# Kernel optimization log

Hardware: AMD Instinct MI355X
Metric: run time of the kernel (lower is better)

The kernel has to match this reference:

```python
import jax, jax.numpy as jnp
import numpy as np

B, N, D, D_A, S, D_K = 512, 8192, 1024, 512, 8, 64

def setup_inputs() -> dict:
    key = jax.random.key(0)
    k1, k2, k3, k4 = jax.random.split(key, 4)
    lecun_q = 1.0 / np.sqrt(D_A)
    lecun_k = 1.0 / np.sqrt(D)
    return {
        "z": jax.random.normal(k1, (B, D_A), dtype=jnp.float32),
        "pool_vectors": jax.random.normal(k2, (N, D), dtype=jnp.float32),
        "W_Q": jax.random.normal(k3, (S, D_A, D_K), dtype=jnp.float32) * lecun_q,
        "W_K": jax.random.normal(k4, (S, D, D_K), dtype=jnp.float32) * lecun_k,
        "aspect_logits": jnp.zeros((S,), dtype=jnp.float32),
        "tau": jnp.asarray(0.5, dtype=jnp.float32),
        "lambda_sharp": jnp.asarray(10.0, dtype=jnp.float32),
        "temperature": jnp.asarray(0.1, dtype=jnp.float32),
    }

def reference(z, pool_vectors, W_Q, W_K, aspect_logits, tau, lambda_sharp, temperature):
    # Per-aspect projections
    queries = jnp.einsum('bd,adq->baq', z, W_Q)              # [B, S, d_k]
    keys = jnp.einsum('np,apq->naq', pool_vectors, W_K)       # [N, S, d_k]
    # L2 normalize along d_k
    q_norm = queries / (jnp.linalg.norm(queries, axis=-1, keepdims=True) + 1e-08)
    k_norm = keys / (jnp.linalg.norm(keys, axis=-1, keepdims=True) + 1e-08)
    # Multi-aspect cosine similarity
    sims = jnp.einsum('baq,naq->bna', q_norm, k_norm)          # [B, N, S]
    # Learned aspect weighting
    w = jax.nn.softmax(aspect_logits)                          # [S]
    scores = jnp.einsum('bna,a->bn', sims, w)                  # [B, N]
    # Sigmoid gate against threshold, temperature-scaled normalize
    g = jax.nn.sigmoid(lambda_sharp * (scores - tau))
    alpha_raw = g * jnp.exp(scores / temperature)
    alpha = alpha_raw / (jnp.sum(alpha_raw, axis=-1, keepdims=True) + 1e-08)
    return (alpha, scores, keys)
```

## Files before the change

kernel.cpp:

```cpp
#include <hip/hip_runtime.h>
#include <stdint.h>

#define B_DIM 512
#define N_DIM 8192
#define D_DIM 1024
#define DA_DIM 512
#define S_DIM 8
#define DK_DIM 64
#define C_DIM 512

typedef short v8s __attribute__((ext_vector_type(8)));
typedef float v4f __attribute__((ext_vector_type(4)));

__device__ __forceinline__ unsigned int f2bf(float x) {
    union { float f; unsigned int u; } v; v.f = x;
    unsigned int u = v.u;
    return (u + 0x7fffu + ((u >> 16) & 1u)) >> 16;
}

__device__ __forceinline__ void gld16(const unsigned short* g, unsigned short* l) {
    __builtin_amdgcn_global_load_lds(
        (const __attribute__((address_space(1))) unsigned int*)g,
        (__attribute__((address_space(3))) unsigned int*)l,
        16, 0, 0);
}

__device__ __forceinline__ void cvt8(const float* __restrict__ src,
                                     unsigned short* __restrict__ dst, int t) {
    const float4* s4 = (const float4*)src;
    float4 a = s4[2 * t], b = s4[2 * t + 1];
    uint4 o;
    o.x = f2bf(a.x) | (f2bf(a.y) << 16);
    o.y = f2bf(a.z) | (f2bf(a.w) << 16);
    o.z = f2bf(b.x) | (f2bf(b.y) << 16);
    o.w = f2bf(b.z) | (f2bf(b.w) << 16);
    ((uint4*)dst)[t] = o;
}

__device__ __forceinline__ void w_transpose(const float* __restrict__ w,
                                            unsigned short* __restrict__ wt,
                                            int c, int ddim) {
    int a = c >> 6, k = c & 63;
    const float* src = w + (size_t)a * ddim * DK_DIM + k;
    unsigned short* drow = wt + (size_t)c * ddim;
    for (int d = threadIdx.x; d < ddim; d += 256)
        drow[d] = (unsigned short)f2bf(src[(size_t)d * DK_DIM]);
}

__global__ __launch_bounds__(256) void prep(const float* __restrict__ pool,
                                            const float* __restrict__ z,
                                            const float* __restrict__ W_Q,
                                            const float* __restrict__ W_K,
                                            unsigned short* __restrict__ poolb,
                                            unsigned short* __restrict__ zb,
                                            unsigned short* __restrict__ wqt,
                                            unsigned short* __restrict__ wtb) {
    int blk = blockIdx.x;
    if (blk < 4096) {
        cvt8(pool, poolb, blk * 256 + threadIdx.x);
    } else if (blk < 4224) {
        cvt8(z, zb, (blk - 4096) * 256 + threadIdx.x);
    } else if (blk < 4736) {
        w_transpose(W_K, wtb, blk - 4224, D_DIM);
    } else {
        w_transpose(W_Q, wqt, blk - 4736, DA_DIM);
    }
}

__device__ __forceinline__ void gemm_mainloop(const unsigned short* __restrict__ A, int lda,
                                              const unsigned short* __restrict__ Bm, int ldb,
                                              int mbase, int nbase, int kiters,
                                              unsigned short* As, unsigned short* Bs,
                                              v4f acc[4][4]) {
    int tid = threadIdx.x;
    int wid = tid >> 6, lane = tid & 63;
    int wm = wid >> 1, wn = wid & 1;
    int quad = lane >> 4, l16 = lane & 15;
    int srow = lane >> 2;
    int scol = (lane & 3) * 8;

    for (int kk = 0; kk < kiters; kk++) {
        #pragma unroll
        for (int j = 0; j < 2; j++) {
            int rgrp = wid * 2 + j;
            int row = rgrp * 16 + srow;
            gld16(&A[(size_t)(mbase + row) * lda + kk * 32 + scol], &As[rgrp * 512]);
            gld16(&Bm[(size_t)(nbase + row) * ldb + kk * 32 + scol], &Bs[rgrp * 512]);
        }
        __syncthreads();
        v8s af[4], bf[4];
        #pragma unroll
        for (int mt = 0; mt < 4; mt++)
            af[mt] = *(const v8s*)&As[(wm * 64 + mt * 16 + l16) * 32 + quad * 8];
        #pragma unroll
        for (int nt = 0; nt < 4; nt++)
            bf[nt] = *(const v8s*)&Bs[(wn * 64 + nt * 16 + l16) * 32 + quad * 8];
        #pragma unroll
        for (int mt = 0; mt < 4; mt++)
            #pragma unroll
            for (int nt = 0; nt < 4; nt++)
                acc[mt][nt] = __builtin_amdgcn_mfma_f32_16x16x32_bf16(
                    af[mt], bf[nt], acc[mt][nt], 0, 0, 0);
        __syncthreads();
    }
}

__global__ __launch_bounds__(256) void fused_gemms(const unsigned short* __restrict__ poolb,
                                                   const unsigned short* __restrict__ wtb,
                                                   const unsigned short* __restrict__ zb,
                                                   const unsigned short* __restrict__ wqt,
                                                   const float* __restrict__ logits,
                                                   float* __restrict__ keys_out,
                                                   unsigned short* __restrict__ kb,
                                                   unsigned short* __restrict__ qwb) {
    __shared__ unsigned short As[4096], Bs[4096];
    v4f acc[4][4];
    #pragma unroll
    for (int mt = 0; mt < 4; mt++)
        #pragma unroll
        for (int nt = 0; nt < 4; nt++) acc[mt][nt] = (v4f)(0.f);

    int blk = blockIdx.x;
    bool is_q = blk >= 256;
    const unsigned short* A;
    const unsigned short* Bm;
    int lda, mbase, nbase, kiters;
    if (is_q) {
        int q = blk - 256;
        A = zb; Bm = wqt; lda = DA_DIM; kiters = DA_DIM / 32;
        mbase = (q >> 2) * 128; nbase = (q & 3) * 128;
    } else {
        A = poolb; Bm = wtb; lda = D_DIM; kiters = D_DIM / 32;
        mbase = (blk >> 2) * 128; nbase = (blk & 3) * 128;
    }

    gemm_mainloop(A, lda, Bm, lda, mbase, nbase, kiters, As, Bs, acc);

    int tid = threadIdx.x, wid = tid >> 6, lane = tid & 63;
    int wm = wid >> 1, wn = wid & 1, quad = lane >> 4, l16 = lane & 15;

    if (is_q) {
        float l[8]; float mx = -1e30f;
        #pragma unroll
        for (int i = 0; i < 8; i++) { l[i] = logits[i]; mx = fmaxf(mx, l[i]); }
        float se = 0.f;
        #pragma unroll
        for (int i = 0; i < 8; i++) { l[i] = __expf(l[i] - mx); se += l[i]; }
        float wa = l[(nbase >> 6) + wn] / se;

        #pragma unroll
        for (int mt = 0; mt < 4; mt++)
            #pragma unroll
            for (int r = 0; r < 4; r++) {
                float ss = 0.f;
                #pragma unroll
                for (int nt = 0; nt < 4; nt++) {
                    float s = acc[mt][nt][r];
                    ss += s * s;
                }
                ss += __shfl_xor(ss, 1, 64);
                ss += __shfl_xor(ss, 2, 64);
                ss += __shfl_xor(ss, 4, 64);
                ss += __shfl_xor(ss, 8, 64);
                float sc = wa / (sqrtf(ss) + 1e-8f);
                int row = mbase + wm * 64 + mt * 16 + quad * 4 + r;
                #pragma unroll
                for (int nt = 0; nt < 4; nt++) {
                    int col = nbase + wn * 64 + nt * 16 + l16;
                    qwb[(size_t)row * C_DIM + col] =
                        (unsigned short)f2bf(acc[mt][nt][r] * sc);
                }
            }
    } else {
        #pragma unroll
        for (int mt = 0; mt < 4; mt++)
            #pragma unroll
            for (int r = 0; r < 4; r++) {
                float ss = 0.f;
                #pragma unroll
                for (int nt = 0; nt < 4; nt++) {
                    float s = acc[mt][nt][r];
                    ss += s * s;
                }
                ss += __shfl_xor(ss, 1, 64);
                ss += __shfl_xor(ss, 2, 64);
                ss += __shfl_xor(ss, 4, 64);
                ss += __shfl_xor(ss, 8, 64);
                float sc = 1.0f / (sqrtf(ss) + 1e-8f);
                int row = mbase + wm * 64 + mt * 16 + quad * 4 + r;
                #pragma unroll
                for (int nt = 0; nt < 4; nt++) {
                    int col = nbase + wn * 64 + nt * 16 + l16;
                    float s = acc[mt][nt][r];
                    keys_out[(size_t)row * C_DIM + col] = s;
                    kb[(size_t)row * C_DIM + col] = (unsigned short)f2bf(s * sc);
                }
            }
    }
}

__global__ __launch_bounds__(256) void scores_gemm(const unsigned short* __restrict__ qwb,
                                                   const unsigned short* __restrict__ kb,
                                                   float* __restrict__ scores_out,
                                                   float* __restrict__ partials,
                                                   const float* __restrict__ lam_p,
                                                   const float* __restrict__ tau_p,
                                                   const float* __restrict__ temp_p) {
    __shared__ unsigned short As[4096], Bs[4096];
    __shared__ float rowpart[128];
    v4f acc[4][4];
    #pragma unroll
    for (int mt = 0; mt < 4; mt++)
        #pragma unroll
        for (int nt = 0; nt < 4; nt++) acc[mt][nt] = (v4f)(0.f);

    int mbase = blockIdx.y * 128, nbase = blockIdx.x * 128;
    gemm_mainloop(qwb, C_DIM, kb, C_DIM, mbase, nbase, C_DIM / 32, As, Bs, acc);

    int tid = threadIdx.x, wid = tid >> 6, lane = tid & 63;
    int wm = wid >> 1, wn = wid & 1, quad = lane >> 4, l16 = lane & 15;

    if (tid < 128) rowpart[tid] = 0.f;
    __syncthreads();

    float lam = lam_p[0], tau = tau_p[0], invT = 1.0f / temp_p[0];
    float rsum[4][4];
    #pragma unroll
    for (int mt = 0; mt < 4; mt++)
        #pragma unroll
        for (int r = 0; r < 4; r++) rsum[mt][r] = 0.f;

    #pragma unroll
    for (int mt = 0; mt < 4; mt++)
        #pragma unroll
        for (int nt = 0; nt < 4; nt++)
            #pragma unroll
            for (int r = 0; r < 4; r++) {
                float s = acc[mt][nt][r];
                int row = mbase + wm * 64 + mt * 16 + quad * 4 + r;
                int col = nbase + wn * 64 + nt * 16 + l16;
                scores_out[(size_t)row * N_DIM + col] = s;
                float g = 1.0f / (1.0f + __expf(-lam * (s - tau)));
                rsum[mt][r] += g * __expf(s * invT);
            }
    #pragma unroll
    for (int mt = 0; mt < 4; mt++)
        #pragma unroll
        for (int r = 0; r < 4; r++) {
            float v = rsum[mt][r];
            v += __shfl_xor(v, 1, 64);
            v += __shfl_xor(v, 2, 64);
            v += __shfl_xor(v, 4, 64);
            v += __shfl_xor(v, 8, 64);
            if (l16 == 0)
                atomicAdd(&rowpart[wm * 64 + mt * 16 + quad * 4 + r], v);
        }
    __syncthreads();
    if (tid < 128)
        partials[(size_t)blockIdx.x * B_DIM + mbase + tid] = rowpart[tid];
}

__global__ __launch_bounds__(256) void alpha_kernel(const float* __restrict__ scores,
                                                    const float* __restrict__ partials,
                                                    float* __restrict__ alpha,
                                                    const float* __restrict__ lam_p,
                                                    const float* __restrict__ tau_p,
                                                    const float* __restrict__ temp_p) {
    __shared__ float s_inv;
    int b = blockIdx.x;
    int tid = threadIdx.x;
    if (tid < 64) {
        float v = partials[(size_t)tid * B_DIM + b];
        v += __shfl_xor(v, 1, 64);
        v += __shfl_xor(v, 2, 64);
        v += __shfl_xor(v, 4, 64);
        v += __shfl_xor(v, 8, 64);
        v += __shfl_xor(v, 16, 64);
        v += __shfl_xor(v, 32, 64);
        if (tid == 0) s_inv = 1.0f / (v + 1e-8f);
    }
    __syncthreads();
    float inv = s_inv;
    float lam = lam_p[0], tau = tau_p[0], invT = 1.0f / temp_p[0];
    const float4* srow = (const float4*)(scores + (size_t)b * N_DIM);
    float4* arow = (float4*)(alpha + (size_t)b * N_DIM);
    #pragma unroll
    for (int i = 0; i < 8; i++) {
        int idx = tid + i * 256;
        float4 s4 = srow[idx];
        float4 o;
        o.x = (1.0f / (1.0f + __expf(-lam * (s4.x - tau)))) * __expf(s4.x * invT) * inv;
        o.y = (1.0f / (1.0f + __expf(-lam * (s4.y - tau)))) * __expf(s4.y * invT) * inv;
        o.z = (1.0f / (1.0f + __expf(-lam * (s4.z - tau)))) * __expf(s4.z * invT) * inv;
        o.w = (1.0f / (1.0f + __expf(-lam * (s4.w - tau)))) * __expf(s4.w * invT) * inv;
        arow[idx] = o;
    }
}

extern "C" void kernel_launch(void* const* d_in, const int* in_sizes, int n_in,
                              void* d_out, int out_size, void* d_ws, size_t ws_size,
                              hipStream_t stream) {
    const float* z      = (const float*)d_in[0];
    const float* pool   = (const float*)d_in[1];
    const float* W_Q    = (const float*)d_in[2];
    const float* W_K    = (const float*)d_in[3];
    const float* logits = (const float*)d_in[4];
    const float* tau    = (const float*)d_in[5];
    const float* lam    = (const float*)d_in[6];
    const float* temp   = (const float*)d_in[7];

    float* alpha  = (float*)d_out;
    float* scores = alpha + (size_t)B_DIM * N_DIM;
    float* keys   = scores + (size_t)B_DIM * N_DIM;

    char* ws = (char*)d_ws;
    unsigned short* poolb = (unsigned short*)(ws);
    unsigned short* kb    = (unsigned short*)(ws + 16777216);
    unsigned short* wtb   = (unsigned short*)(ws + 25165824);
    unsigned short* wqt   = (unsigned short*)(ws + 26214400);
    unsigned short* zb    = (unsigned short*)(ws + 26738688);
    unsigned short* qwb   = (unsigned short*)(ws + 27262976);
    float* partials       = (float*)(ws + 27787264);

    prep<<<dim3(5248), dim3(256), 0, stream>>>(pool, z, W_Q, W_K,
                                               poolb, zb, wqt, wtb);
    fused_gemms<<<dim3(272), dim3(256), 0, stream>>>(poolb, wtb, zb, wqt, logits,
                                                     keys, kb, qwb);
    scores_gemm<<<dim3(64, 4), dim3(256), 0, stream>>>(qwb, kb, scores, partials,
                                                       lam, tau, temp);
    alpha_kernel<<<dim3(512), dim3(256), 0, stream>>>(scores, partials, alpha,
                                                      lam, tau, temp);
}
```

Baseline: 161.2 us.

## Double-buffer GEMM LDS tiles and use tiled shared-memory weight transpose

The GEMM main loop now double-buffers its A/B shared-memory tiles, issuing the next k-slice's global-to-LDS loads before computing on the current slice, with one barrier per iteration instead of two. The weight transpose in the prep kernel becomes a 64x64 tiled transpose through padded shared memory, so global reads and writes are coalesced instead of strided, and the transpose grid shrinks. This doubles GEMM LDS usage, which may lower occupancy. The single barrier per iteration relies on the buffer being overwritten having been consumed in the previous iteration.

```diff
diff --git a/kernel.cpp b/kernel.cpp
--- a/kernel.cpp
+++ b/kernel.cpp
@@ -37,14 +37,39 @@
     ((uint4*)dst)[t] = o;
 }
 
-__device__ __forceinline__ void w_transpose(const float* __restrict__ w,
-                                            unsigned short* __restrict__ wt,
-                                            int c, int ddim) {
-    int a = c >> 6, k = c & 63;
-    const float* src = w + (size_t)a * ddim * DK_DIM + k;
-    unsigned short* drow = wt + (size_t)c * ddim;
-    for (int d = threadIdx.x; d < ddim; d += 256)
-        drow[d] = (unsigned short)f2bf(src[(size_t)d * DK_DIM]);
+__device__ __forceinline__ void w_transpose_tile(const float* __restrict__ w,
+                                                 unsigned short* __restrict__ wt,
+                                                 int a, int dt, int ddim,
+                                                 unsigned short* T ) {
+    int t = threadIdx.x;
+    int d0 = dt * 64;
+    int kc4 = (t & 15) * 4;
+    const float4* src = (const float4*)(w + ((size_t)a * ddim + d0) * DK_DIM);
+    #pragma unroll
+    for (int p = 0; p < 4; p++) {
+        int dr = p * 16 + (t >> 4);
+        float4 v = src[dr * 16 + (t & 15)];
+        uint2 pk;
+        pk.x = f2bf(v.x) | (f2bf(v.y) << 16);
+        pk.y = f2bf(v.z) | (f2bf(v.w) << 16);
+        *(uint2*)&T[dr * 68 + kc4] = pk;
+    }
+    __syncthreads();
+    int c0 = a * 64;
+    #pragma unroll
+    for (int q = 0; q < 2; q++) {
+        int k = q * 32 + (t >> 3);
+        int ch = t & 7;
+        unsigned short s[8];
+        #pragma unroll
+        for (int i = 0; i < 8; i++) s[i] = T[(ch * 8 + i) * 68 + k];
+        uint4 o;
+        o.x = (unsigned)s[0] | ((unsigned)s[1] << 16);
+        o.y = (unsigned)s[2] | ((unsigned)s[3] << 16);
+        o.z = (unsigned)s[4] | ((unsigned)s[5] << 16);
+        o.w = (unsigned)s[6] | ((unsigned)s[7] << 16);
+        *(uint4*)&wt[(size_t)(c0 + k) * ddim + d0 + ch * 8] = o;
+    }
 }
 
 __global__ __launch_bounds__(256) void prep(const float* __restrict__ pool,
@@ -55,22 +80,26 @@
                                             unsigned short* __restrict__ zb,
                                             unsigned short* __restrict__ wqt,
                                             unsigned short* __restrict__ wtb) {
+    __shared__ unsigned short T[64 * 68];
     int blk = blockIdx.x;
     if (blk < 4096) {
         cvt8(pool, poolb, blk * 256 + threadIdx.x);
     } else if (blk < 4224) {
         cvt8(z, zb, (blk - 4096) * 256 + threadIdx.x);
-    } else if (blk < 4736) {
-        w_transpose(W_K, wtb, blk - 4224, D_DIM);
+    } else if (blk < 4352) {
+        int idx = blk - 4224;
+        w_transpose_tile(W_K, wtb, idx >> 4, idx & 15, D_DIM, T);
     } else {
-        w_transpose(W_Q, wqt, blk - 4736, DA_DIM);
+        int idx = blk - 4352;
+        w_transpose_tile(W_Q, wqt, idx >> 3, idx & 7, DA_DIM, T);
     }
 }
 
 __device__ __forceinline__ void gemm_mainloop(const unsigned short* __restrict__ A, int lda,
                                               const unsigned short* __restrict__ Bm, int ldb,
                                               int mbase, int nbase, int kiters,
-                                              unsigned short* As, unsigned short* Bs,
+                                              unsigned short (*As)[4096],
+                                              unsigned short (*Bs)[4096],
                                               v4f acc[4][4]) {
     int tid = threadIdx.x;
     int wid = tid >> 6, lane = tid & 63;
@@ -79,29 +108,34 @@
     int srow = lane >> 2;
     int scol = (lane & 3) * 8;
 
-    for (int kk = 0; kk < kiters; kk++) {
+    auto stage = [&](int kk, int p) {
         #pragma unroll
         for (int j = 0; j < 2; j++) {
             int rgrp = wid * 2 + j;
             int row = rgrp * 16 + srow;
-            gld16(&A[(size_t)(mbase + row) * lda + kk * 32 + scol], &As[rgrp * 512]);
-            gld16(&Bm[(size_t)(nbase + row) * ldb + kk * 32 + scol], &Bs[rgrp * 512]);
+            gld16(&A[(size_t)(mbase + row) * lda + kk * 32 + scol], &As[p][rgrp * 512]);
+            gld16(&Bm[(size_t)(nbase + row) * ldb + kk * 32 + scol], &Bs[p][rgrp * 512]);
         }
+    };
+
+    stage(0, 0);
+    for (int kk = 0; kk < kiters; kk++) {
         __syncthreads();
+        if (kk + 1 < kiters) stage(kk + 1, (kk + 1) & 1);
+        int p = kk & 1;
         v8s af[4], bf[4];
         #pragma unroll
         for (int mt = 0; mt < 4; mt++)
-            af[mt] = *(const v8s*)&As[(wm * 64 + mt * 16 + l16) * 32 + quad * 8];
+            af[mt] = *(const v8s*)&As[p][(wm * 64 + mt * 16 + l16) * 32 + quad * 8];
         #pragma unroll
         for (int nt = 0; nt < 4; nt++)
-            bf[nt] = *(const v8s*)&Bs[(wn * 64 + nt * 16 + l16) * 32 + quad * 8];
+            bf[nt] = *(const v8s*)&Bs[p][(wn * 64 + nt * 16 + l16) * 32 + quad * 8];
         #pragma unroll
         for (int mt = 0; mt < 4; mt++)
             #pragma unroll
             for (int nt = 0; nt < 4; nt++)
                 acc[mt][nt] = __builtin_amdgcn_mfma_f32_16x16x32_bf16(
                     af[mt], bf[nt], acc[mt][nt], 0, 0, 0);
-        __syncthreads();
     }
 }
 
@@ -113,7 +147,7 @@
                                                    float* __restrict__ keys_out,
                                                    unsigned short* __restrict__ kb,
                                                    unsigned short* __restrict__ qwb) {
-    __shared__ unsigned short As[4096], Bs[4096];
+    __shared__ unsigned short As[2][4096], Bs[2][4096];
     v4f acc[4][4];
     #pragma unroll
     for (int mt = 0; mt < 4; mt++)
@@ -154,10 +188,7 @@
             for (int r = 0; r < 4; r++) {
                 float ss = 0.f;
                 #pragma unroll
-                for (int nt = 0; nt < 4; nt++) {
-                    float s = acc[mt][nt][r];
-                    ss += s * s;
-                }
+                for (int nt = 0; nt < 4; nt++) ss += acc[mt][nt][r] * acc[mt][nt][r];
                 ss += __shfl_xor(ss, 1, 64);
                 ss += __shfl_xor(ss, 2, 64);
                 ss += __shfl_xor(ss, 4, 64);
@@ -178,10 +209,7 @@
             for (int r = 0; r < 4; r++) {
                 float ss = 0.f;
                 #pragma unroll
-                for (int nt = 0; nt < 4; nt++) {
-                    float s = acc[mt][nt][r];
-                    ss += s * s;
-                }
+                for (int nt = 0; nt < 4; nt++) ss += acc[mt][nt][r] * acc[mt][nt][r];
                 ss += __shfl_xor(ss, 1, 64);
                 ss += __shfl_xor(ss, 2, 64);
                 ss += __shfl_xor(ss, 4, 64);
@@ -206,7 +234,7 @@
                                                    const float* __restrict__ lam_p,
                                                    const float* __restrict__ tau_p,
                                                    const float* __restrict__ temp_p) {
-    __shared__ unsigned short As[4096], Bs[4096];
+    __shared__ unsigned short As[2][4096], Bs[2][4096];
     __shared__ float rowpart[128];
     v4f acc[4][4];
     #pragma unroll
@@ -322,7 +350,7 @@
     unsigned short* qwb   = (unsigned short*)(ws + 27262976);
     float* partials       = (float*)(ws + 27787264);
 
-    prep<<<dim3(5248), dim3(256), 0, stream>>>(pool, z, W_Q, W_K,
+    prep<<<dim3(4416), dim3(256), 0, stream>>>(pool, z, W_Q, W_K,
                                                poolb, zb, wqt, wtb);
     fused_gemms<<<dim3(272), dim3(256), 0, stream>>>(poolb, wtb, zb, wqt, logits,
                                                      keys, kb, qwb);
```

New measurement: 157.9 us. -2.1%, faster.
